# Kernel optimization log

Measured on AMD Instinct MI355X. Metric: run time of the kernel, lower is better.

The kernel has to match this reference:

```python
import jax, jax.numpy as jnp
import numpy as np

P, B, L = 32, 64, 128
E, HB, HP = 64, 128, 128   # byte emb dim, byte GRU hidden, packet GRU hidden
PE = 2 * HB                # packet embedding dim = 256
LH = 128                   # attention linear hidden
NC = 10                    # num classes


def _gru_dir(x, w_ih, w_hh, b_ih, b_hh, reverse=False):
    # x: [T, N, E_in] -> outputs [T, N, H]; PyTorch GRU gate math, h0 = 0.
    H = w_hh.shape[1]
    xg = jnp.einsum('tne,ge->tng', x, w_ih) + b_ih  # precompute input gates [T,N,3H]
    if reverse:
        xg = xg[::-1]

    def step(h, xgt):
        hg = h @ w_hh.T + b_hh
        xr, xz, xn = jnp.split(xgt, 3, axis=-1)
        hr, hz, hn = jnp.split(hg, 3, axis=-1)
        r = jax.nn.sigmoid(xr + hr)
        z = jax.nn.sigmoid(xz + hz)
        n = jnp.tanh(xn + r * hn)
        h = (1.0 - z) * n + z * h
        return h, h

    h0 = jnp.zeros((x.shape[1], H), x.dtype)
    _, ys = jax.lax.scan(step, h0, xg)
    if reverse:
        ys = ys[::-1]
    return ys


def _bigru(x, wif, whf, bif, bhf, wib, whb, bib, bhb):
    f = _gru_dir(x, wif, whf, bif, bhf, reverse=False)
    b = _gru_dir(x, wib, whb, bib, bhb, reverse=True)
    return jnp.concatenate([f, b], axis=-1)


def setup_inputs() -> dict:
    key = jax.random.key(0)
    ks = jax.random.split(key, 32)
    rn = lambda k, shp: (jax.random.normal(k, shp, dtype=jnp.float32) * 0.05)
    inp = {}
    inp['flow'] = jax.random.randint(ks[0], (P, B, L), 0, 256, dtype=jnp.int64)
    inp['emb'] = rn(ks[1], (256, E))
    # byte biGRU (forward / backward dirs)
    inp['byte_wih_f'] = rn(ks[2], (3 * HB, E)); inp['byte_whh_f'] = rn(ks[3], (3 * HB, HB))
    inp['byte_bih_f'] = rn(ks[4], (3 * HB,));   inp['byte_bhh_f'] = rn(ks[5], (3 * HB,))
    inp['byte_wih_b'] = rn(ks[6], (3 * HB, E)); inp['byte_whh_b'] = rn(ks[7], (3 * HB, HB))
    inp['byte_bih_b'] = rn(ks[8], (3 * HB,));   inp['byte_bhh_b'] = rn(ks[9], (3 * HB,))
    # packet biGRU
    inp['pkt_wih_f'] = rn(ks[10], (3 * HP, PE)); inp['pkt_whh_f'] = rn(ks[11], (3 * HP, HP))
    inp['pkt_bih_f'] = rn(ks[12], (3 * HP,));    inp['pkt_bhh_f'] = rn(ks[13], (3 * HP,))
    inp['pkt_wih_b'] = rn(ks[14], (3 * HP, PE)); inp['pkt_whh_b'] = rn(ks[15], (3 * HP, HP))
    inp['pkt_bih_b'] = rn(ks[16], (3 * HP,));    inp['pkt_bhh_b'] = rn(ks[17], (3 * HP,))
    # byte attention (Linear(2HB->LH), Linear(LH->1))
    inp['ba_w1'] = rn(ks[18], (LH, 2 * HB)); inp['ba_b1'] = rn(ks[19], (LH,))
    inp['ba_w2'] = rn(ks[20], (1, LH));      inp['ba_b2'] = rn(ks[21], (1,))
    # packet attention (Linear(2HP->LH), Linear(LH->1))
    inp['pa_w1'] = rn(ks[22], (LH, 2 * HP)); inp['pa_b1'] = rn(ks[23], (LH,))
    inp['pa_w2'] = rn(ks[24], (1, LH));      inp['pa_b2'] = rn(ks[25], (1,))
    # final classifier
    inp['wf'] = rn(ks[26], (NC, 2 * HP)); inp['bf'] = rn(ks[27], (NC,))
    return inp


def reference(flow, emb,
              byte_wih_f, byte_whh_f, byte_bih_f, byte_bhh_f,
              byte_wih_b, byte_whh_b, byte_bih_b, byte_bhh_b,
              pkt_wih_f, pkt_whh_f, pkt_bih_f, pkt_bhh_f,
              pkt_wih_b, pkt_whh_b, pkt_bih_b, pkt_bhh_b,
              ba_w1, ba_b1, ba_w2, ba_b2,
              pa_w1, pa_b1, pa_w2, pa_b2,
              wf, bf):
    p, b, l = flow.shape
    x = emb[flow]                                   # [P,B,L,E]
    # batch the per-packet byte GRU across packets: [L, P*B, E]
    xb = x.transpose(2, 0, 1, 3).reshape(l, p * b, E)
    out = _bigru(xb, byte_wih_f, byte_whh_f, byte_bih_f, byte_bhh_f,
                 byte_wih_b, byte_whh_b, byte_bih_b, byte_bhh_b)  # [L, P*B, 2HB]
    out = out.reshape(l, p, b, 2 * HB)
    # Attention: tanh(lin1) -> lin2 -> softmax over dim=1 of the [L,B,1] view,
    # i.e. over the batch axis (faithful to the original code).
    h = jnp.tanh(jnp.einsum('lpbd,hd->lpbh', out, ba_w1) + ba_b1)
    score = jnp.einsum('lpbh,oh->lpbo', h, ba_w2) + ba_b2          # [L,P,B,1]
    attn = jax.nn.softmax(score, axis=2)
    packet_emb = (out * attn).sum(axis=0)                          # [P,B,2HB]
    # packet biGRU over packet sequence
    out2 = _bigru(packet_emb, pkt_wih_f, pkt_whh_f, pkt_bih_f, pkt_bhh_f,
                  pkt_wih_b, pkt_whh_b, pkt_bih_b, pkt_bhh_b)      # [P,B,2HP]
    h2 = jnp.tanh(jnp.einsum('pbd,hd->pbh', out2, pa_w1) + pa_b1)
    score2 = jnp.einsum('pbh,oh->pbo', h2, pa_w2) + pa_b2          # [P,B,1]
    attn2 = jax.nn.softmax(score2, axis=1)
    flow_emb = (out2 * attn2).sum(axis=1)                          # [P,2HP] (faithful sum over dim=1)
    return flow_emb @ wf.T + bf                                    # [P,NC]
```

## Files before the change

### kernel.cpp

```cpp
#include <hip/hip_runtime.h>
#include <hip/hip_bf16.h>
#include <hip/hip_fp16.h>
#include <cstdint>
#include <cstddef>


#define DINLINE __device__ __forceinline__

typedef _Float16 f16;
typedef f16 f16x8 __attribute__((ext_vector_type(8)));
typedef float f32x4 __attribute__((ext_vector_type(4)));

#define SCL_RZ (-1.44269504089f)
#define SCL_N (2.88539008178f)

static DINLINE float fast_tanh(float x) {
    const float e = __builtin_amdgcn_exp2f(2.88539008178f * x);
    return 1.0f - 2.0f * __builtin_amdgcn_rcpf(1.0f + e);
}

static DINLINE void lds_barrier() {
    asm volatile("s_waitcnt lgkmcnt(0)\n\ts_barrier" ::: "memory");
    __builtin_amdgcn_sched_barrier(0);
}

__global__ void k_tables_w1(const float* __restrict__ emb,
                            const float* __restrict__ wihF, const float* __restrict__ bihF,
                            const float* __restrict__ bhhF,
                            const float* __restrict__ wihB, const float* __restrict__ bihB,
                            const float* __restrict__ bhhB,
                            float4* __restrict__ tab4F, float4* __restrict__ tab4B,
                            const float* __restrict__ w1, f16* __restrict__ w1h,
                            const float* __restrict__ pwihF, const float* __restrict__ pwihB,
                            float* __restrict__ wihTpF, float* __restrict__ wihTpB) {
    if (blockIdx.x >= 640) {
        const int bid = blockIdx.x - 640;
        const int m = bid / 96, bx = bid % 96;
        const float* __restrict__ s = m ? pwihB : pwihF;
        float* __restrict__ d = m ? wihTpB : wihTpF;
        for (int idx = bx * 384 + threadIdx.x; idx < 384 * 256; idx += 96 * 384) {
            const int r = idx >> 8, c = idx & 255;
            d[c * 384 + r] = s[idx];
        }
        return;
    }
    if (blockIdx.x >= 512) {
        const int col = blockIdx.x - 512;
        const int k = threadIdx.x;
        if (k < 256)
            w1h[col * 256 + (k ^ ((col & 7) << 3))] =
                (f16)(SCL_N * w1[col * 256 + k]);
        return;
    }
    const int v = blockIdx.x & 255;
    const int dir = blockIdx.x >> 8;
    const float* wih = dir ? wihB : wihF;
    const float* bih = dir ? bihB : bihF;
    const float* bhh = dir ? bhhB : bhhF;
    float4* tab4 = dir ? tab4B : tab4F;
    __shared__ float er[64];
    __shared__ float sh[384];
    if (threadIdx.x < 64) er[threadIdx.x] = emb[v * 64 + threadIdx.x];
    __syncthreads();
    const int g = threadIdx.x;
    float acc = bih[g] + (g < 256 ? bhh[g] : 0.0f);
    #pragma unroll
    for (int e = 0; e < 64; ++e) acc = fmaf(wih[g * 64 + e], er[e], acc);
    sh[g] = acc * (g < 256 ? SCL_RZ : SCL_N);
    __syncthreads();
    if (g < 128) {
        float4 pk;
        pk.x = sh[g];
        pk.y = sh[g + 128];
        pk.z = sh[g + 256];
        pk.w = 0.f;
        tab4[v * 128 + g] = pk;
    }
}

__global__ __launch_bounds__(512, 1) void k_byte_gru(
    const int* __restrict__ flow,
    const float4* __restrict__ tab4F, const float4* __restrict__ tab4B,
    const float* __restrict__ whhF, const float* __restrict__ whhB,
    const float* __restrict__ bhhF, const float* __restrict__ bhhB,
    __half* __restrict__ hF, __half* __restrict__ hB) {
    const int dir = blockIdx.x & 1;
    const int chunk = blockIdx.x >> 1;
    const int row0 = chunk * 16;
    const int tid = threadIdx.x;
    const int wid = tid >> 6;
    const int lane = tid & 63;
    const int c = lane & 15;
    const int q = lane >> 4;
    const int j = wid * 16 + c;

    const char* __restrict__ t4j =
        reinterpret_cast<const char*>(dir ? tab4B : tab4F) + (j << 4);
    const float* __restrict__ whh = dir ? whhB : whhF;
    const float* __restrict__ bhh = dir ? bhhB : bhhF;
    __half* __restrict__ hout = dir ? hB : hF;

    __shared__ f16 hbuf[2][16 * 128];
    __shared__ int flow_lds[128][16];

    for (int i = tid; i < 16 * 128; i += 512) {
        const int row = i >> 7, t = i & 127;
        flow_lds[t][row] = (flow[row0 * 128 + i] & 255) << 11;
    }
    for (int i = tid; i < 16 * 128; i += 512) hbuf[0][i] = (f16)0.f;

    f16x8 Bf[3][4];
    #pragma unroll
    for (int g = 0; g < 3; ++g) {
        const float scl = (g == 2) ? SCL_N : SCL_RZ;
        #pragma unroll
        for (int ks = 0; ks < 4; ++ks) {
            const float* src = whh + (size_t)(g * 128 + j) * 128 + ks * 32 + q * 8;
            f16x8 b;
            #pragma unroll
            for (int e = 0; e < 8; ++e) b[e] = (f16)(scl * src[e]);
            Bf[g][ks] = b;
        }
    }
    const float bh2 = SCL_N * bhh[j + 256];
    float hold[4];
    #pragma unroll
    for (int rr = 0; rr < 4; ++rr) hold[rr] = 0.f;
    __syncthreads();

    for (int t = 0; t < 128; ++t) {
        const int curb = t & 1, nxtb = curb ^ 1;
        const int tt = dir ? (127 - t) : t;

        const int4 off4 = *reinterpret_cast<const int4*>(&flow_lds[tt][q * 4]);
        float4 x4[4];
        x4[0] = *reinterpret_cast<const float4*>(t4j + off4.x);
        x4[1] = *reinterpret_cast<const float4*>(t4j + off4.y);
        x4[2] = *reinterpret_cast<const float4*>(t4j + off4.z);
        x4[3] = *reinterpret_cast<const float4*>(t4j + off4.w);

        f16x8 Af[4];
        #pragma unroll
        for (int ks = 0; ks < 4; ++ks) {
            const int kb = ks * 32 + q * 8;
            const int idx = c * 128 + (kb ^ ((c & 7) << 3));
            Af[ks] = *reinterpret_cast<const f16x8*>(&hbuf[curb][idx]);
        }

        f32x4 a0 = {0.f, 0.f, 0.f, 0.f};
        f32x4 a1 = {0.f, 0.f, 0.f, 0.f};
        f32x4 a2 = {0.f, 0.f, 0.f, 0.f};
        #pragma unroll
        for (int ks = 0; ks < 4; ++ks) {
            a0 = __builtin_amdgcn_mfma_f32_16x16x32_f16(Af[ks], Bf[0][ks], a0, 0, 0, 0);
            a1 = __builtin_amdgcn_mfma_f32_16x16x32_f16(Af[ks], Bf[1][ks], a1, 0, 0, 0);
            a2 = __builtin_amdgcn_mfma_f32_16x16x32_f16(Af[ks], Bf[2][ks], a2, 0, 0, 0);
        }

        __half* hp = hout + ((size_t)tt * 2048 + row0 + q * 4) * 128 + j;
        #pragma unroll
        for (int rr = 0; rr < 4; ++rr) {
            const float e0 = __builtin_amdgcn_exp2f(x4[rr].x + a0[rr]);
            const float rg = __builtin_amdgcn_rcpf(1.0f + e0);
            const float e1 = __builtin_amdgcn_exp2f(x4[rr].y + a1[rr]);
            const float zg = __builtin_amdgcn_rcpf(1.0f + e1);
            const float e2 =
                __builtin_amdgcn_exp2f(x4[rr].z + rg * (a2[rr] + bh2));
            const float ng = fmaf(-2.0f, __builtin_amdgcn_rcpf(1.0f + e2), 1.0f);
            const float hn = fmaf(zg, hold[rr] - ng, ng);
            hold[rr] = hn;
            const int row = q * 4 + rr;
            hbuf[nxtb][row * 128 + (j ^ ((row & 7) << 3))] = (f16)hn;
            hp[rr * 128] = (__half)hn;
        }
        lds_barrier();
    }
}

__global__ __launch_bounds__(256, 1) void k_scores_attn(
    const __half* __restrict__ hF, const __half* __restrict__ hB,
    const f16* __restrict__ w1h,
    const float* __restrict__ b1, const float* __restrict__ w2,
    const float* __restrict__ b2, float* __restrict__ attn) {
    __shared__ f16 w1lds[128 * 256];
    __shared__ float sc[128];
    const int tid = threadIdx.x;
    {
        const uint2* src = reinterpret_cast<const uint2*>(w1h);
        uint2* dst = reinterpret_cast<uint2*>(w1lds);
        for (int i = tid; i < 8192; i += 256) dst[i] = src[i];
    }
    const int lane = tid & 63, w = tid >> 6;
    const int c = lane & 15, q = lane >> 4;

    float b1v[8], w2v[8];
    #pragma unroll
    for (int ct = 0; ct < 8; ++ct) {
        b1v[ct] = SCL_N * b1[ct * 16 + c];
        w2v[ct] = w2[ct * 16 + c];
    }
    const float b2v = b2[0];
    __syncthreads();

    for (int it = 0; it < 2; ++it) {
        const int pos0 = blockIdx.x * 256 + it * 128;

        f16x8 Af[2][8];
        #pragma unroll
        for (int pt = 0; pt < 2; ++pt) {
            const size_t pos = (size_t)pos0 + (w * 2 + pt) * 16 + c;
            const f16* hFp = (const f16*)(hF + pos * 128);
            const f16* hBp = (const f16*)(hB + pos * 128);
            #pragma unroll
            for (int ks = 0; ks < 4; ++ks)
                Af[pt][ks] = *reinterpret_cast<const f16x8*>(hFp + ks * 32 + q * 8);
            #pragma unroll
            for (int ks = 0; ks < 4; ++ks)
                Af[pt][4 + ks] = *reinterpret_cast<const f16x8*>(hBp + ks * 32 + q * 8);
        }

        float s[2][4] = {{0.f, 0.f, 0.f, 0.f}, {0.f, 0.f, 0.f, 0.f}};
        #pragma unroll
        for (int ct = 0; ct < 8; ++ct) {
            const int jj = ct * 16 + c;
            f16x8 Bfr[8];
            #pragma unroll
            for (int ks = 0; ks < 8; ++ks) {
                const int k = ks * 32 + q * 8;
                Bfr[ks] = *reinterpret_cast<const f16x8*>(
                    &w1lds[jj * 256 + (k ^ ((jj & 7) << 3))]);
            }
            #pragma unroll
            for (int pt = 0; pt < 2; ++pt) {
                f32x4 acc = {0.f, 0.f, 0.f, 0.f};
                #pragma unroll
                for (int ks = 0; ks < 8; ++ks)
                    acc = __builtin_amdgcn_mfma_f32_16x16x32_f16(Af[pt][ks],
                                                                 Bfr[ks], acc,
                                                                 0, 0, 0);
                #pragma unroll
                for (int rr = 0; rr < 4; ++rr) {
                    const float e2 = __builtin_amdgcn_exp2f(acc[rr] + b1v[ct]);
                    const float th =
                        fmaf(-2.0f, __builtin_amdgcn_rcpf(1.0f + e2), 1.0f);
                    s[pt][rr] = fmaf(w2v[ct], th, s[pt][rr]);
                }
            }
        }
        #pragma unroll
        for (int pt = 0; pt < 2; ++pt) {
            #pragma unroll
            for (int rr = 0; rr < 4; ++rr) {
                float v = s[pt][rr];
                v += __shfl_xor(v, 1);
                v += __shfl_xor(v, 2);
                v += __shfl_xor(v, 4);
                v += __shfl_xor(v, 8);
                if (c == 0) sc[(w * 2 + pt) * 16 + q * 4 + rr] = v + b2v;
            }
        }
        __syncthreads();
        if (tid < 128) {
            const float sv = sc[tid];
            float m = sv;
            for (int off = 32; off; off >>= 1) m = fmaxf(m, __shfl_xor(m, off));
            const float e = __expf(sv - m);
            float sum = e;
            for (int off = 32; off; off >>= 1) sum += __shfl_xor(sum, off);
            attn[pos0 + tid] = e / sum;
        }
        __syncthreads();
    }
}

__global__ __launch_bounds__(256) void k_packet_emb(
    const __half* __restrict__ hF, const __half* __restrict__ hB,
    const float* __restrict__ attn, float* __restrict__ pe) {
    const int tid = threadIdx.x;
    const int g = tid >> 6;
    const int lane = tid & 63;
    const int n = blockIdx.x * 4 + g;
    const bool isF = lane < 32;
    const int chunk = lane & 31;
    const __half* __restrict__ hsrc = (isF ? hF : hB) + (size_t)n * 128 + chunk * 4;
    float acc0 = 0.f, acc1 = 0.f, acc2 = 0.f, acc3 = 0.f;
    for (int l0 = 0; l0 < 128; l0 += 8) {
        float wv[8];
        uint2 u[8];
        #pragma unroll
        for (int k = 0; k < 8; ++k) {
            wv[k] = attn[(l0 + k) * 2048 + n];
            u[k] = *reinterpret_cast<const uint2*>(hsrc +
                                                   (size_t)(l0 + k) * 2048 * 128);
        }
        #pragma unroll
        for (int k = 0; k < 8; ++k) {
            const f16* hv = reinterpret_cast<const f16*>(&u[k]);
            acc0 = fmaf(wv[k], (float)hv[0], acc0);
            acc1 = fmaf(wv[k], (float)hv[1], acc1);
            acc2 = fmaf(wv[k], (float)hv[2], acc2);
            acc3 = fmaf(wv[k], (float)hv[3], acc3);
        }
    }
    float4 o = {acc0, acc1, acc2, acc3};
    *reinterpret_cast<float4*>(&pe[n * 256 + (isF ? 0 : 128) + chunk * 4]) = o;
}

__global__ __launch_bounds__(384) void k_pkt_xg(
    const float* __restrict__ pe, const float* __restrict__ wihTF,
    const float* __restrict__ bihF, const float* __restrict__ bhhF,
    const float* __restrict__ wihTB, const float* __restrict__ bihB,
    const float* __restrict__ bhhB, float4* __restrict__ xg4F,
    float4* __restrict__ xg4B) {
    const int dir = blockIdx.y;
    const float* __restrict__ wihT = dir ? wihTB : wihTF;
    const float* __restrict__ bih = dir ? bihB : bihF;
    const float* __restrict__ bhh = dir ? bhhB : bhhF;
    float4* __restrict__ xg4 = dir ? xg4B : xg4F;
    const int rbase = blockIdx.x * 8;
    __shared__ float xrow[8][256];
    __shared__ float sh[8][384];
    for (int i = threadIdx.x; i < 8 * 256; i += 384)
        xrow[i >> 8][i & 255] = pe[rbase * 256 + i];
    __syncthreads();
    const int g = threadIdx.x;
    float acc[8];
    const float bias = bih[g] + (g < 256 ? bhh[g] : 0.0f);
    #pragma unroll
    for (int r = 0; r < 8; ++r) acc[r] = bias;
    for (int d = 0; d < 256; ++d) {
        const float w = wihT[d * 384 + g];
        #pragma unroll
        for (int r = 0; r < 8; ++r) acc[r] = fmaf(w, xrow[r][d], acc[r]);
    }
    const float scl = (g < 256) ? SCL_RZ : SCL_N;
    #pragma unroll
    for (int r = 0; r < 8; ++r) sh[r][g] = scl * acc[r];
    __syncthreads();
    for (int i = threadIdx.x; i < 8 * 128; i += 384) {
        const int r = i >> 7, jj = i & 127;
        float4 pk;
        pk.x = sh[r][jj];
        pk.y = sh[r][jj + 128];
        pk.z = sh[r][jj + 256];
        pk.w = 0.f;
        xg4[(size_t)(rbase + r) * 128 + jj] = pk;
    }
}

__global__ __launch_bounds__(512, 1) void k_pkt_gru(
    const float4* __restrict__ xg4F, const float4* __restrict__ xg4B,
    const float* __restrict__ whhF, const float* __restrict__ whhB,
    const float* __restrict__ bhhF, const float* __restrict__ bhhB,
    float* __restrict__ h2F, float* __restrict__ h2B) {
    const int dir = blockIdx.x & 1;
    const int chunk = blockIdx.x >> 1;
    const int row0 = chunk * 16;
    const int tid = threadIdx.x;
    const int wid = tid >> 6;
    const int lane = tid & 63;
    const int c = lane & 15;
    const int q = lane >> 4;
    const int j = wid * 16 + c;

    const float4* __restrict__ xg4 = dir ? xg4B : xg4F;
    const float* __restrict__ whh = dir ? whhB : whhF;
    const float* __restrict__ bhh = dir ? bhhB : bhhF;
    float* __restrict__ hout = dir ? h2B : h2F;

    __shared__ f16 hbuf[2][16 * 128];

    for (int i = tid; i < 16 * 128; i += 512) hbuf[0][i] = (f16)0.f;

    f16x8 Bf[3][4];
    #pragma unroll
    for (int g = 0; g < 3; ++g) {
        const float scl = (g == 2) ? SCL_N : SCL_RZ;
        #pragma unroll
        for (int ks = 0; ks < 4; ++ks) {
            const float* src = whh + (size_t)(g * 128 + j) * 128 + ks * 32 + q * 8;
            f16x8 b;
            #pragma unroll
            for (int e = 0; e < 8; ++e) b[e] = (f16)(scl * src[e]);
            Bf[g][ks] = b;
        }
    }
    const float bh2 = SCL_N * bhh[j + 256];
    float hold[4];
    #pragma unroll
    for (int rr = 0; rr < 4; ++rr) hold[rr] = 0.f;
    __syncthreads();

    for (int t = 0; t < 32; ++t) {
        const int curb = t & 1, nxtb = curb ^ 1;
        const int tt = dir ? (31 - t) : t;

        float4 x4[4];
        #pragma unroll
        for (int rr = 0; rr < 4; ++rr)
            x4[rr] = xg4[(size_t)(tt * 64 + row0 + q * 4 + rr) * 128 + j];

        f16x8 Af[4];
        #pragma unroll
        for (int ks = 0; ks < 4; ++ks) {
            const int kb = ks * 32 + q * 8;
            const int idx = c * 128 + (kb ^ ((c & 7) << 3));
            Af[ks] = *reinterpret_cast<const f16x8*>(&hbuf[curb][idx]);
        }

        f32x4 a0 = {0.f, 0.f, 0.f, 0.f};
        f32x4 a1 = {0.f, 0.f, 0.f, 0.f};
        f32x4 a2 = {0.f, 0.f, 0.f, 0.f};
        #pragma unroll
        for (int ks = 0; ks < 4; ++ks) {
            a0 = __builtin_amdgcn_mfma_f32_16x16x32_f16(Af[ks], Bf[0][ks], a0, 0, 0, 0);
            a1 = __builtin_amdgcn_mfma_f32_16x16x32_f16(Af[ks], Bf[1][ks], a1, 0, 0, 0);
            a2 = __builtin_amdgcn_mfma_f32_16x16x32_f16(Af[ks], Bf[2][ks], a2, 0, 0, 0);
        }

        #pragma unroll
        for (int rr = 0; rr < 4; ++rr) {
            const float e0 = __builtin_amdgcn_exp2f(x4[rr].x + a0[rr]);
            const float rg = __builtin_amdgcn_rcpf(1.0f + e0);
            const float e1 = __builtin_amdgcn_exp2f(x4[rr].y + a1[rr]);
            const float zg = __builtin_amdgcn_rcpf(1.0f + e1);
            const float e2 =
                __builtin_amdgcn_exp2f(x4[rr].z + rg * (a2[rr] + bh2));
            const float ng = fmaf(-2.0f, __builtin_amdgcn_rcpf(1.0f + e2), 1.0f);
            const float hn = fmaf(zg, hold[rr] - ng, ng);
            hold[rr] = hn;
            const int row = q * 4 + rr;
            hbuf[nxtb][row * 128 + (j ^ ((row & 7) << 3))] = (f16)hn;
            hout[((size_t)tt * 64 + row0 + row) * 128 + j] = hn;
        }
        lds_barrier();
    }
}

__global__ __launch_bounds__(128) void k_scores2(
    const float* __restrict__ h2F, const float* __restrict__ h2B,
    const float* __restrict__ paw1,
    const float* __restrict__ pab1, const float* __restrict__ paw2,
    const float* __restrict__ pab2, float* __restrict__ scores2) {
    const int n = blockIdx.x;
    const int tid = threadIdx.x;
    __shared__ float x[256];
    __shared__ float red[2];
    x[tid] = h2F[n * 128 + tid];
    x[tid + 128] = h2B[n * 128 + tid];
    __syncthreads();
    float acc = pab1[tid];
    const float* wr = paw1 + tid * 256;
    #pragma unroll 8
    for (int d = 0; d < 256; ++d) acc = fmaf(wr[d], x[d], acc);
    float s = paw2[tid] * fast_tanh(acc);
    s += __shfl_xor(s, 1);
    s += __shfl_xor(s, 2);
    s += __shfl_xor(s, 4);
    s += __shfl_xor(s, 8);
    s += __shfl_xor(s, 16);
    s += __shfl_xor(s, 32);
    if ((tid & 63) == 0) red[tid >> 6] = s;
    __syncthreads();
    if (tid == 0) scores2[n] = red[0] + red[1] + pab2[0];
}

__global__ __launch_bounds__(256) void k_final3(
    const float* __restrict__ h2F, const float* __restrict__ h2B,
    const float* __restrict__ scores2, const float* __restrict__ wf,
    const float* __restrict__ bfv, float* __restrict__ outp) {
    const int p = blockIdx.x;
    const int tid = threadIdx.x;
    __shared__ float sc[64];
    __shared__ float femb[256];
    __shared__ float red[64];

    if (tid < 64) {
        const float s = scores2[p * 64 + tid];
        float m = s;
        for (int off = 32; off; off >>= 1) m = fmaxf(m, __shfl_xor(m, off));
        const float e = __expf(s - m);
        float sum = e;
        for (int off = 32; off; off >>= 1) sum += __shfl_xor(sum, off);
        sc[tid] = e / sum;
    }
    __syncthreads();

    {
        const float* __restrict__ hsrc = (tid < 128) ? h2F : h2B;
        const int d = tid & 127;
        float acc = 0.f;
        for (int b = 0; b < 64; ++b)
            acc = fmaf(sc[b], hsrc[(p * 64 + b) * 128 + d], acc);
        femb[tid] = acc;
    }
    __syncthreads();

    const float fv = femb[tid];
    #pragma unroll
    for (int c = 0; c < 10; ++c) {
        float s = fv * wf[c * 256 + tid];
        s += __shfl_xor(s, 1);
        s += __shfl_xor(s, 2);
        s += __shfl_xor(s, 4);
        s += __shfl_xor(s, 8);
        s += __shfl_xor(s, 16);
        s += __shfl_xor(s, 32);
        if ((tid & 63) == 0) red[(c << 2) | (tid >> 6)] = s;
        __syncthreads();
        if (tid == 0)
            outp[p * 10 + c] = bfv[c] + red[c << 2] + red[(c << 2) | 1] +
                               red[(c << 2) | 2] + red[(c << 2) | 3];
        __syncthreads();
    }
}

extern "C" void kernel_launch(void* const* d_in, const int* in_sizes, int n_in,
                              void* d_out, int out_size, void* d_ws,
                              size_t ws_size, hipStream_t stream) {
    const int* flow = (const int*)d_in[0];
    const float* emb = (const float*)d_in[1];
    const float* byte_wih_f = (const float*)d_in[2];
    const float* byte_whh_f = (const float*)d_in[3];
    const float* byte_bih_f = (const float*)d_in[4];
    const float* byte_bhh_f = (const float*)d_in[5];
    const float* byte_wih_b = (const float*)d_in[6];
    const float* byte_whh_b = (const float*)d_in[7];
    const float* byte_bih_b = (const float*)d_in[8];
    const float* byte_bhh_b = (const float*)d_in[9];
    const float* pkt_wih_f = (const float*)d_in[10];
    const float* pkt_whh_f = (const float*)d_in[11];
    const float* pkt_bih_f = (const float*)d_in[12];
    const float* pkt_bhh_f = (const float*)d_in[13];
    const float* pkt_wih_b = (const float*)d_in[14];
    const float* pkt_whh_b = (const float*)d_in[15];
    const float* pkt_bih_b = (const float*)d_in[16];
    const float* pkt_bhh_b = (const float*)d_in[17];
    const float* ba_w1 = (const float*)d_in[18];
    const float* ba_b1 = (const float*)d_in[19];
    const float* ba_w2 = (const float*)d_in[20];
    const float* ba_b2 = (const float*)d_in[21];
    const float* pa_w1 = (const float*)d_in[22];
    const float* pa_b1 = (const float*)d_in[23];
    const float* pa_w2 = (const float*)d_in[24];
    const float* pa_b2 = (const float*)d_in[25];
    const float* wf = (const float*)d_in[26];
    const float* bf = (const float*)d_in[27];

    char* base = (char*)d_ws;
    size_t off = 0;
    auto allocf = [&](size_t nf) -> float* {
        float* p = (float*)(base + off);
        off += nf * sizeof(float);
        return p;
    };
    auto alloch = [&](size_t nh) -> __half* {
        off = (off + 255) & ~(size_t)255;
        __half* p = (__half*)(base + off);
        off += nh * sizeof(__half);
        return p;
    };
    float* wihTpF = allocf(256 * 384);
    float* wihTpB = allocf(256 * 384);
    float* attn = allocf(262144);
    float* pe = allocf(2048 * 256);
    float4* tab4F = (float4*)allocf(256 * 128 * 4);
    float4* tab4B = (float4*)allocf(256 * 128 * 4);
    float4* xg4F = (float4*)allocf((size_t)2048 * 128 * 4);
    float4* xg4B = (float4*)allocf((size_t)2048 * 128 * 4);
    float* h2F = allocf(32 * 64 * 128);
    float* h2B = allocf(32 * 64 * 128);
    float* scores2 = allocf(2048);
    __half* w1h = alloch(128 * 256);
    __half* hF = alloch((size_t)128 * 2048 * 128);
    __half* hB = alloch((size_t)128 * 2048 * 128);
    if (off > ws_size) return;
    (void)in_sizes; (void)n_in; (void)out_size;

    k_tables_w1<<<832, 384, 0, stream>>>(emb, byte_wih_f, byte_bih_f,
                                         byte_bhh_f, byte_wih_b, byte_bih_b,
                                         byte_bhh_b, tab4F, tab4B, ba_w1,
                                         (f16*)w1h, pkt_wih_f, pkt_wih_b,
                                         wihTpF, wihTpB);

    k_byte_gru<<<256, 512, 0, stream>>>(flow, tab4F, tab4B, byte_whh_f,
                                        byte_whh_b, byte_bhh_f, byte_bhh_b, hF,
                                        hB);

    k_scores_attn<<<1024, 256, 0, stream>>>(hF, hB, (const f16*)w1h, ba_b1,
                                            ba_w2, ba_b2, attn);
    k_packet_emb<<<512, 256, 0, stream>>>(hF, hB, attn, pe);

    k_pkt_xg<<<dim3(256, 2), 384, 0, stream>>>(pe, wihTpF, pkt_bih_f,
                                               pkt_bhh_f, wihTpB, pkt_bih_b,
                                               pkt_bhh_b, xg4F, xg4B);
    k_pkt_gru<<<8, 512, 0, stream>>>(xg4F, xg4B, pkt_whh_f, pkt_whh_b,
                                     pkt_bhh_f, pkt_bhh_b, h2F, h2B);
    k_scores2<<<2048, 128, 0, stream>>>(h2F, h2B, pa_w1, pa_b1, pa_w2, pa_b2,
                                        scores2);
    k_final3<<<32, 256, 0, stream>>>(h2F, h2B, scores2, wf, bf, (float*)d_out);
}
```

Before: 282.5 us.

## Spread packet GRU and packet embedding over more blocks, hoist byte GRU output pointer

The packet GRU now gives each block 4 batch rows instead of 16. It launches 32 blocks instead of 8, with only the first row of each 4-row MFMA group carrying real data (the rest stay zero). This shortens the serial per-step epilogue and spreads the latency-bound recurrence over more CUs, at the cost of mostly wasted MFMA work. The packet-embedding reduction splits the sequence across two waves and combines them through shared memory with twice as many blocks, and the byte GRU output pointer is advanced incrementally instead of recomputed each step.

```diff
diff --git a/kernel.cpp b/kernel.cpp
--- a/kernel.cpp
+++ b/kernel.cpp
@@ -126,6 +126,10 @@
     float hold[4];
     #pragma unroll
     for (int rr = 0; rr < 4; ++rr) hold[rr] = 0.f;
+
+    const int tt0 = dir ? 127 : 0;
+    __half* hp = hout + ((size_t)tt0 * 2048 + row0 + q * 4) * 128 + j;
+    const ptrdiff_t hstep = (dir ? -1 : 1) * (ptrdiff_t)2048 * 128;
     __syncthreads();
 
     for (int t = 0; t < 128; ++t) {
@@ -157,7 +161,6 @@
             a2 = __builtin_amdgcn_mfma_f32_16x16x32_f16(Af[ks], Bf[2][ks], a2, 0, 0, 0);
         }
 
-        __half* hp = hout + ((size_t)tt * 2048 + row0 + q * 4) * 128 + j;
         #pragma unroll
         for (int rr = 0; rr < 4; ++rr) {
             const float e0 = __builtin_amdgcn_exp2f(x4[rr].x + a0[rr]);
@@ -173,6 +176,7 @@
             hbuf[nxtb][row * 128 + (j ^ ((row & 7) << 3))] = (f16)hn;
             hp[rr * 128] = (__half)hn;
         }
+        hp += hstep;
         lds_barrier();
     }
 }
@@ -277,21 +281,22 @@
     const __half* __restrict__ hF, const __half* __restrict__ hB,
     const float* __restrict__ attn, float* __restrict__ pe) {
     const int tid = threadIdx.x;
-    const int g = tid >> 6;
+    const int w = tid >> 6;
     const int lane = tid & 63;
-    const int n = blockIdx.x * 4 + g;
+    const int n = blockIdx.x * 2 + (w >> 1);
+    const int l0 = (w & 1) * 64;
     const bool isF = lane < 32;
     const int chunk = lane & 31;
     const __half* __restrict__ hsrc = (isF ? hF : hB) + (size_t)n * 128 + chunk * 4;
     float acc0 = 0.f, acc1 = 0.f, acc2 = 0.f, acc3 = 0.f;
-    for (int l0 = 0; l0 < 128; l0 += 8) {
+    for (int lb = 0; lb < 64; lb += 8) {
         float wv[8];
         uint2 u[8];
         #pragma unroll
         for (int k = 0; k < 8; ++k) {
-            wv[k] = attn[(l0 + k) * 2048 + n];
-            u[k] = *reinterpret_cast<const uint2*>(hsrc +
-                                                   (size_t)(l0 + k) * 2048 * 128);
+            const int l = l0 + lb + k;
+            wv[k] = attn[l * 2048 + n];
+            u[k] = *reinterpret_cast<const uint2*>(hsrc + (size_t)l * 2048 * 128);
         }
         #pragma unroll
         for (int k = 0; k < 8; ++k) {
@@ -302,8 +307,15 @@
             acc3 = fmaf(wv[k], (float)hv[3], acc3);
         }
     }
-    float4 o = {acc0, acc1, acc2, acc3};
-    *reinterpret_cast<float4*>(&pe[n * 256 + (isF ? 0 : 128) + chunk * 4]) = o;
+    __shared__ float4 part[4][64];
+    part[w][lane] = (float4){acc0, acc1, acc2, acc3};
+    __syncthreads();
+    if ((w & 1) == 0) {
+        const float4 a = part[w][lane];
+        const float4 b = part[w + 1][lane];
+        float4 o = {a.x + b.x, a.y + b.y, a.z + b.z, a.w + b.w};
+        *reinterpret_cast<float4*>(&pe[n * 256 + (isF ? 0 : 128) + chunk * 4]) = o;
+    }
 }
 
 __global__ __launch_bounds__(384) void k_pkt_xg(
@@ -355,7 +367,7 @@
     float* __restrict__ h2F, float* __restrict__ h2B) {
     const int dir = blockIdx.x & 1;
     const int chunk = blockIdx.x >> 1;
-    const int row0 = chunk * 16;
+    const int row0 = chunk * 4;
     const int tid = threadIdx.x;
     const int wid = tid >> 6;
     const int lane = tid & 63;
@@ -370,7 +382,10 @@
 
     __shared__ f16 hbuf[2][16 * 128];
 
-    for (int i = tid; i < 16 * 128; i += 512) hbuf[0][i] = (f16)0.f;
+    {
+        f16* hb = reinterpret_cast<f16*>(hbuf);
+        for (int i = tid; i < 2 * 16 * 128; i += 512) hb[i] = (f16)0.f;
+    }
 
     f16x8 Bf[3][4];
     #pragma unroll
@@ -386,19 +401,15 @@
         }
     }
     const float bh2 = SCL_N * bhh[j + 256];
-    float hold[4];
-    #pragma unroll
-    for (int rr = 0; rr < 4; ++rr) hold[rr] = 0.f;
+    float hold = 0.f;
+    const int slot = q * 4;
     __syncthreads();
 
     for (int t = 0; t < 32; ++t) {
         const int curb = t & 1, nxtb = curb ^ 1;
         const int tt = dir ? (31 - t) : t;
 
-        float4 x4[4];
-        #pragma unroll
-        for (int rr = 0; rr < 4; ++rr)
-            x4[rr] = xg4[(size_t)(tt * 64 + row0 + q * 4 + rr) * 128 + j];
+        const float4 x4 = xg4[(size_t)(tt * 64 + row0 + q) * 128 + j];
 
         f16x8 Af[4];
         #pragma unroll
@@ -418,20 +429,17 @@
             a2 = __builtin_amdgcn_mfma_f32_16x16x32_f16(Af[ks], Bf[2][ks], a2, 0, 0, 0);
         }
 
-        #pragma unroll
-        for (int rr = 0; rr < 4; ++rr) {
-            const float e0 = __builtin_amdgcn_exp2f(x4[rr].x + a0[rr]);
+        {
+            const float e0 = __builtin_amdgcn_exp2f(x4.x + a0[0]);
             const float rg = __builtin_amdgcn_rcpf(1.0f + e0);
-            const float e1 = __builtin_amdgcn_exp2f(x4[rr].y + a1[rr]);
+            const float e1 = __builtin_amdgcn_exp2f(x4.y + a1[0]);
             const float zg = __builtin_amdgcn_rcpf(1.0f + e1);
-            const float e2 =
-                __builtin_amdgcn_exp2f(x4[rr].z + rg * (a2[rr] + bh2));
+            const float e2 = __builtin_amdgcn_exp2f(x4.z + rg * (a2[0] + bh2));
             const float ng = fmaf(-2.0f, __builtin_amdgcn_rcpf(1.0f + e2), 1.0f);
-            const float hn = fmaf(zg, hold[rr] - ng, ng);
-            hold[rr] = hn;
-            const int row = q * 4 + rr;
-            hbuf[nxtb][row * 128 + (j ^ ((row & 7) << 3))] = (f16)hn;
-            hout[((size_t)tt * 64 + row0 + row) * 128 + j] = hn;
+            const float hn = fmaf(zg, hold - ng, ng);
+            hold = hn;
+            hbuf[nxtb][slot * 128 + (j ^ ((slot & 7) << 3))] = (f16)hn;
+            hout[((size_t)tt * 64 + row0 + q) * 128 + j] = hn;
         }
         lds_barrier();
     }
@@ -589,13 +597,13 @@
 
     k_scores_attn<<<1024, 256, 0, stream>>>(hF, hB, (const f16*)w1h, ba_b1,
                                             ba_w2, ba_b2, attn);
-    k_packet_emb<<<512, 256, 0, stream>>>(hF, hB, attn, pe);
+    k_packet_emb<<<1024, 256, 0, stream>>>(hF, hB, attn, pe);
 
     k_pkt_xg<<<dim3(256, 2), 384, 0, stream>>>(pe, wihTpF, pkt_bih_f,
                                                pkt_bhh_f, wihTpB, pkt_bih_b,
                                                pkt_bhh_b, xg4F, xg4B);
-    k_pkt_gru<<<8, 512, 0, stream>>>(xg4F, xg4B, pkt_whh_f, pkt_whh_b,
-                                     pkt_bhh_f, pkt_bhh_b, h2F, h2B);
+    k_pkt_gru<<<32, 512, 0, stream>>>(xg4F, xg4B, pkt_whh_f, pkt_whh_b,
+                                      pkt_bhh_f, pkt_bhh_b, h2F, h2B);
     k_scores2<<<2048, 128, 0, stream>>>(h2F, h2B, pa_w1, pa_b1, pa_w2, pa_b2,
                                         scores2);
     k_final3<<<32, 256, 0, stream>>>(h2F, h2B, scores2, wf, bf, (float*)d_out);
```

After: 273.8 us, median of 2. -3.1%, faster.
